# Kernel tuning notes

Measured on AMD Instinct MI355X. Metric: run time of the kernel, lower is better.

## Reference

```python
import jax, jax.numpy as jnp
import numpy as np

B, NV, NQ, NA = 128, 100, 14, 10
V_DIM, Q_DIM, A_DIM = 2048, 1024, 1024
H_DIM, RANK, HD, G = 512, 32, 16, 2  # HD = H_DIM // RANK, G = glimpse


def setup_inputs() -> dict:
    key = jax.random.key(0)
    ks = jax.random.split(key, 16)
    s = 0.05
    return {
        "v": jax.random.normal(ks[0], (B, NV, V_DIM), jnp.float32),
        "q": jax.random.normal(ks[1], (B, NQ, Q_DIM), jnp.float32),
        "a": jax.random.normal(ks[2], (B, NA, A_DIM), jnp.float32),
        # tucker projections (FCNet = Linear + ReLU; dropout identity at eval)
        "Wv": jax.random.normal(ks[3], (H_DIM, V_DIM), jnp.float32) * s,
        "bv": jnp.zeros((H_DIM,), jnp.float32),
        "Wq": jax.random.normal(ks[4], (H_DIM, Q_DIM), jnp.float32) * s,
        "bq": jnp.zeros((H_DIM,), jnp.float32),
        "Wa": jax.random.normal(ks[5], (H_DIM, A_DIM), jnp.float32) * s,
        "ba": jnp.zeros((H_DIM,), jnp.float32),
        # rank-wise projection nets, stacked over rank: [rank, HD, H_DIM]
        "Wvr": jax.random.normal(ks[6], (RANK, HD, H_DIM), jnp.float32) * s,
        "bvr": jnp.zeros((RANK, HD), jnp.float32),
        "Wqr": jax.random.normal(ks[7], (RANK, HD, H_DIM), jnp.float32) * s,
        "bqr": jnp.zeros((RANK, HD), jnp.float32),
        "War": jax.random.normal(ks[8], (RANK, HD, H_DIM), jnp.float32) * s,
        "bar": jnp.zeros((RANK, HD), jnp.float32),
        # Tucker core T_g with h_out squeezed: [rank, hv, hq, ha, glimpse]
        "T": jax.random.normal(ks[9], (RANK, HD, HD, HD, G), jnp.float32),
    }


def reference(v, q, a, Wv, bv, Wq, bq, Wa, ba, Wvr, bvr, Wqr, bqr, War, bar, T):
    relu = jax.nn.relu
    # modality tucker projections: [B, N, H_DIM]
    vt = relu(jnp.einsum('bnd,hd->bnh', v, Wv) + bv)
    qt = relu(jnp.einsum('bnd,hd->bnh', q, Wq) + bq)
    at = relu(jnp.einsum('bnd,hd->bnh', a, Wa) + ba)
    # rank-wise FCNets, batched over rank: [B, rank, N, HD]
    v_ = relu(jnp.einsum('bnh,rch->brnc', vt, Wvr) + bvr[None, :, None, :])
    q_ = relu(jnp.einsum('bnh,rch->brnc', qt, Wqr) + bqr[None, :, None, :])
    a_ = relu(jnp.einsum('bnh,rch->brnc', at, War) + bar[None, :, None, :])
    # 6-way Tucker contraction, summed over rank: [B, NV, NQ, NA, G]
    f_emb = jnp.einsum('rijkg,bnvi,bnqj,bnak->bvqag', T, v_, q_, a_,
                       optimize=True)
    return f_emb
```

## Files before the change

### kernel.cpp

```cpp
#include <hip/hip_runtime.h>
#include <cstddef>
#include <cstdint>

#define B_    128
#define NV_   100
#define NQ_   14
#define NA_   10
#define HDIM  512
#define RANK_ 32
#define HD_   16
#define G_    2

typedef __bf16 bf16x8 __attribute__((ext_vector_type(8)));
typedef float  f32x4  __attribute__((ext_vector_type(4)));
union Frag { uint4 u; bf16x8 v; };

__device__ __forceinline__ unsigned int f2bf(float f) {
  unsigned int u = __float_as_uint(f);
  u = (u + 0x7FFFu + ((u >> 16) & 1u)) >> 16;
  return u & 0xFFFFu;
}

__device__ __forceinline__ void gload_lds16(const unsigned short* gp,
                                            unsigned short* dp) {
  __builtin_amdgcn_global_load_lds(
      (const __attribute__((address_space(1))) void*)gp,
      (__attribute__((address_space(3))) void*)dp, 16, 0, 0);
}

__global__ __launch_bounds__(256) void cvt_kernel(
    const float* __restrict__ s0, const float* __restrict__ s1,
    const float* __restrict__ s2, const float* __restrict__ s3,
    const float* __restrict__ s4, const float* __restrict__ s5,
    const float* __restrict__ s6, const float* __restrict__ s7,
    unsigned short* __restrict__ dst)
{
  const int pref[8] = {896, 1536, 2048, 2304, 2560, 2688, 2816, 2944};
  const float* srcs[8] = {s0, s1, s2, s3, s4, s5, s6, s7};
  const int blk = blockIdx.x;
  int seg = 0;
  #pragma unroll
  for (int i = 0; i < 7; ++i) if (blk >= pref[i]) seg = i + 1;
  const int base_chunk = seg ? pref[seg - 1] : 0;
  const size_t loc = (size_t)(blk - base_chunk) * 2048 + threadIdx.x * 8;
  const float* s = srcs[seg] + loc;
  float4 f0 = *(const float4*)s;
  float4 f1 = *(const float4*)(s + 4);
  ushort4 o0, o1;
  o0.x = f2bf(f0.x); o0.y = f2bf(f0.y); o0.z = f2bf(f0.z); o0.w = f2bf(f0.w);
  o1.x = f2bf(f1.x); o1.y = f2bf(f1.y); o1.z = f2bf(f1.z); o1.w = f2bf(f1.w);
  unsigned short* d = dst + (size_t)blk * 2048 + threadIdx.x * 8;
  *(ushort4*)d = o0;
  *(ushort4*)(d + 4) = o1;
}

__device__ __forceinline__ void stage_swz8(const unsigned short* __restrict__ src,
                                           int K, unsigned short* dst, int t)
{
  const int wb = t & 448;
  const int l = t & 63;
  #pragma unroll
  for (int i = 0; i < 2; ++i) {
    const int sb = i * 512 + wb;
    const int li = sb + l;
    const int row = li >> 3;
    const int p = li & 7;
    const int s = p ^ (row & 7);
    gload_lds16(src + (size_t)row * K + s * 8, dst + sb * 8);
  }
}

__device__ __forceinline__ void cvt_write(const float4 f[4], unsigned short* Abuf,
                                          int ar, int kq)
{
  unsigned short* base = Abuf + ar * 64;
  #pragma unroll
  for (int j = 0; j < 2; ++j) {
    uint4 p;
    p.x = f2bf(f[2*j].x)   | (f2bf(f[2*j].y)   << 16);
    p.y = f2bf(f[2*j].z)   | (f2bf(f[2*j].w)   << 16);
    p.z = f2bf(f[2*j+1].x) | (f2bf(f[2*j+1].y) << 16);
    p.w = f2bf(f[2*j+1].z) | (f2bf(f[2*j+1].w) << 16);
    const int s = (kq * 2 + j) ^ (ar & 7);
    *(uint4*)&base[s * 8] = p;
  }
}

__global__ __launch_bounds__(512, 4) void l1_gemm(
    const float* __restrict__ v,
    const unsigned short* __restrict__ qb, const unsigned short* __restrict__ ab,
    const unsigned short* __restrict__ Wvb, const unsigned short* __restrict__ Wqb,
    const unsigned short* __restrict__ Wab,
    const float* __restrict__ bv, const float* __restrict__ bq,
    const float* __restrict__ ba,
    unsigned short* __restrict__ vtb, unsigned short* __restrict__ qtb,
    unsigned short* __restrict__ atb)
{
  __shared__ __align__(16) unsigned short As[2][8192];
  __shared__ __align__(16) unsigned short Bs[2][8192];
  const int bx = blockIdx.x;
  int grp, gx, gy, K;
  const unsigned short *A16 = qb, *W;
  const float* bias;
  unsigned short* C;
  if (bx < 400) {
    grp = 0; const int xcd = bx & 7, j = bx >> 3; const int m = xcd * 50 + j;
    gy = m >> 2; gx = m & 3; W = Wvb; bias = bv; C = vtb; K = 2048;
  } else if (bx < 456) {
    grp = 1; const int lo = bx - 400; gy = lo >> 2; gx = lo & 3;
    A16 = qb; W = Wqb; bias = bq; C = qtb; K = 1024;
  } else {
    grp = 2; const int lo = bx - 456; gy = lo >> 2; gx = lo & 3;
    A16 = ab; W = Wab; bias = ba; C = atb; K = 1024;
  }
  const int nsteps = K >> 6;
  const int bm = gy * 128, bn = gx * 128;
  const int t = threadIdx.x;
  const int w = t >> 6, l = t & 63;
  const int wm = (w >> 2) * 64, wn = (w & 3) * 32;

  f32x4 acc[4][2];
  #pragma unroll
  for (int i = 0; i < 4; ++i)
    #pragma unroll
    for (int j = 0; j < 2; ++j) acc[i][j] = f32x4{0.f, 0.f, 0.f, 0.f};

  const int ar = t >> 2, kq = t & 3;
  const float* vrow = (grp == 0)
      ? v + (size_t)(bm + ar) * 2048 + kq * 16 : (const float*)nullptr;
  float4 R0[4], R1[4];

  stage_swz8(W + (size_t)bn * K, K, Bs[0], t);
  if (grp == 0) {
    #pragma unroll
    for (int i = 0; i < 4; ++i) R0[i] = ((const float4*)vrow)[i];
    #pragma unroll
    for (int i = 0; i < 4; ++i) R1[i] = ((const float4*)(vrow + 64))[i];
    cvt_write(R0, As[0], ar, kq);
  } else {
    stage_swz8(A16 + (size_t)bm * K, K, As[0], t);
  }
  __syncthreads();

  for (int step = 0; step < nsteps; ++step) {
    const int db = step & 1;
    const bool hn = (step + 1) < nsteps;
    if (hn) stage_swz8(W + (size_t)bn * K + (step + 1) * 64, K, Bs[db ^ 1], t);
    if (grp == 0) {
      if (step + 2 < nsteps) {
        const float* p = vrow + (step + 2) * 64;
        if (db == 0) {
          #pragma unroll
          for (int i = 0; i < 4; ++i) R0[i] = ((const float4*)p)[i];
        } else {
          #pragma unroll
          for (int i = 0; i < 4; ++i) R1[i] = ((const float4*)p)[i];
        }
      }
      if (hn) {
        if (db == 0) cvt_write(R1, As[1], ar, kq);
        else         cvt_write(R0, As[0], ar, kq);
      }
    } else if (hn) {
      stage_swz8(A16 + (size_t)bm * K + (step + 1) * 64, K, As[db ^ 1], t);
    }
    const unsigned short* Ad = As[db];
    const unsigned short* Bd = Bs[db];
    #pragma unroll
    for (int ks = 0; ks < 2; ++ks) {
      Frag fa[4], fb[2];
      #pragma unroll
      for (int i = 0; i < 4; ++i) {
        const int r = wm + 16 * i + (l & 15);
        fa[i].u = *(const uint4*)&Ad[r * 64 + (((ks * 4 + (l >> 4)) ^ (r & 7)) * 8)];
      }
      #pragma unroll
      for (int j = 0; j < 2; ++j) {
        const int r = wn + 16 * j + (l & 15);
        fb[j].u = *(const uint4*)&Bd[r * 64 + (((ks * 4 + (l >> 4)) ^ (r & 7)) * 8)];
      }
      #pragma unroll
      for (int i = 0; i < 4; ++i)
        #pragma unroll
        for (int j = 0; j < 2; ++j)
          acc[i][j] = __builtin_amdgcn_mfma_f32_16x16x32_bf16(fa[i].v, fb[j].v, acc[i][j], 0, 0, 0);
    }
    __syncthreads();
  }

  const int q4 = (l >> 4) * 4, cl = l & 15;
  #pragma unroll
  for (int i = 0; i < 4; ++i)
    #pragma unroll
    for (int j = 0; j < 2; ++j) {
      const int col = bn + wn + 16 * j + cl;
      const float bs = bias[col];
      #pragma unroll
      for (int r = 0; r < 4; ++r) {
        const int row = bm + wm + 16 * i + q4 + r;
        float o = fmaxf(acc[i][j][r] + bs, 0.f);
        C[(size_t)row * 512 + col] = (unsigned short)f2bf(o);
      }
    }
}

__global__ __launch_bounds__(512, 4) void l2_gemm(
    const unsigned short* __restrict__ vtb, const unsigned short* __restrict__ qtb,
    const unsigned short* __restrict__ atb,
    const unsigned short* __restrict__ Wvrb, const unsigned short* __restrict__ Wqrb,
    const unsigned short* __restrict__ Warb,
    const float* __restrict__ bvr, const float* __restrict__ bqr,
    const float* __restrict__ bar,
    unsigned short* __restrict__ vrb, float* __restrict__ q_r, float* __restrict__ a_r)
{
  __shared__ __align__(16) unsigned short As[2][8192];
  __shared__ __align__(16) unsigned short Bs[2][8192];
  const int bx = blockIdx.x;
  int grp, gx, gy;
  const unsigned short *A16, *W;
  const float* bias;
  if (bx < 400) {
    grp = 0; const int xcd = bx & 7, j = bx >> 3; const int m = xcd * 50 + j;
    gy = m >> 2; gx = m & 3; A16 = vtb; W = Wvrb; bias = bvr;
  } else if (bx < 456) {
    grp = 1; const int lo = bx - 400; gy = lo >> 2; gx = lo & 3;
    A16 = qtb; W = Wqrb; bias = bqr;
  } else {
    grp = 2; const int lo = bx - 456; gy = lo >> 2; gx = lo & 3;
    A16 = atb; W = Warb; bias = bar;
  }
  const int bm = gy * 128, bn = gx * 128;
  const int t = threadIdx.x;
  const int w = t >> 6, l = t & 63;
  const int wm = (w >> 2) * 64, wn = (w & 3) * 32;

  f32x4 acc[4][2];
  #pragma unroll
  for (int i = 0; i < 4; ++i)
    #pragma unroll
    for (int j = 0; j < 2; ++j) acc[i][j] = f32x4{0.f, 0.f, 0.f, 0.f};

  stage_swz8(W + (size_t)bn * 512, 512, Bs[0], t);
  stage_swz8(A16 + (size_t)bm * 512, 512, As[0], t);
  __syncthreads();

  for (int step = 0; step < 8; ++step) {
    const int db = step & 1;
    const bool hn = (step + 1) < 8;
    const int k0n = (step + 1) << 6;
    if (hn) {
      stage_swz8(W + (size_t)bn * 512 + k0n, 512, Bs[db ^ 1], t);
      stage_swz8(A16 + (size_t)bm * 512 + k0n, 512, As[db ^ 1], t);
    }
    const unsigned short* Ad = As[db];
    const unsigned short* Bd = Bs[db];
    #pragma unroll
    for (int ks = 0; ks < 2; ++ks) {
      Frag fa[4], fb[2];
      #pragma unroll
      for (int i = 0; i < 4; ++i) {
        const int r = wm + 16 * i + (l & 15);
        fa[i].u = *(const uint4*)&Ad[r * 64 + (((ks * 4 + (l >> 4)) ^ (r & 7)) * 8)];
      }
      #pragma unroll
      for (int j = 0; j < 2; ++j) {
        const int r = wn + 16 * j + (l & 15);
        fb[j].u = *(const uint4*)&Bd[r * 64 + (((ks * 4 + (l >> 4)) ^ (r & 7)) * 8)];
      }
      #pragma unroll
      for (int i = 0; i < 4; ++i)
        #pragma unroll
        for (int j = 0; j < 2; ++j)
          acc[i][j] = __builtin_amdgcn_mfma_f32_16x16x32_bf16(fa[i].v, fb[j].v, acc[i][j], 0, 0, 0);
    }
    __syncthreads();
  }

  const int q4 = (l >> 4) * 4, cl = l & 15;
  #pragma unroll
  for (int i = 0; i < 4; ++i)
    #pragma unroll
    for (int j = 0; j < 2; ++j) {
      const int col = bn + wn + 16 * j + cl;
      const float bs = bias[col];
      #pragma unroll
      for (int r = 0; r < 4; ++r) {
        const int row = bm + wm + 16 * i + q4 + r;
        float o = fmaxf(acc[i][j][r] + bs, 0.f);
        if (grp == 0)      vrb[(size_t)row * 512 + col] = (unsigned short)f2bf(o);
        else if (grp == 1) q_r[(size_t)row * 512 + col] = o;
        else               a_r[(size_t)row * 512 + col] = o;
      }
    }
}

__global__ void tsum_kernel(const float* __restrict__ T, float* __restrict__ Tsum)
{
  const int idx = blockIdx.x * 256 + threadIdx.x;
  float s = 0.f;
  #pragma unroll
  for (int r = 0; r < RANK_; ++r) s += T[r * 8192 + idx];
  Tsum[idx] = s;
}

__global__ __launch_bounds__(256) void build_w_kernel(
    const float* __restrict__ q_, const float* __restrict__ a_,
    const float* __restrict__ Tsum, unsigned short* __restrict__ WmatT)
{
  const int n = blockIdx.x, b = blockIdx.y, t = threadIdx.x;
  __shared__ float Ts[8192];
  __shared__ float U[14 * 544];

  #pragma unroll
  for (int s = 0; s < 8; ++s)
    ((float4*)Ts)[s * 256 + t] = ((const float4*)Tsum)[s * 256 + t];
  __syncthreads();

  {
    const int i = t >> 4, k = t & 15;
    float acc0[NQ_], acc1[NQ_];
    #pragma unroll
    for (int q = 0; q < NQ_; ++q) { acc0[q] = 0.f; acc1[q] = 0.f; }
    const float* qbase = q_ + (size_t)b * NQ_ * HDIM + n * 16;
    #pragma unroll
    for (int j = 0; j < 16; ++j) {
      float2 ts = *(const float2*)&Ts[i * 512 + j * 32 + k * 2];
      #pragma unroll
      for (int q = 0; q < NQ_; ++q) {
        float qv = qbase[q * HDIM + j];
        acc0[q] += ts.x * qv;
        acc1[q] += ts.y * qv;
      }
    }
    #pragma unroll
    for (int q = 0; q < NQ_; ++q) {
      float2 uu; uu.x = acc0[q]; uu.y = acc1[q];
      *(float2*)&U[q * 544 + i * 34 + k * 2] = uu;
    }
  }
  __syncthreads();

  if ((t >> 4) < NQ_) {
    const int q = t >> 4, i = t & 15;
    float acc0[NA_], acc1[NA_];
    #pragma unroll
    for (int a = 0; a < NA_; ++a) { acc0[a] = 0.f; acc1[a] = 0.f; }
    const float* abase = a_ + (size_t)b * NA_ * HDIM + n * 16;
    #pragma unroll
    for (int k = 0; k < 16; ++k) {
      float2 uu = *(const float2*)&U[q * 544 + i * 34 + k * 2];
      #pragma unroll
      for (int a = 0; a < NA_; ++a) {
        float av = abase[a * HDIM + k];
        acc0[a] += uu.x * av;
        acc1[a] += uu.y * av;
      }
    }
    unsigned short* wb = WmatT + (size_t)b * 320 * 512 + (n * 16 + i);
    #pragma unroll
    for (int a = 0; a < NA_; ++a) {
      wb[(size_t)((q * 10 + a) * 2 + 0) * 512] = (unsigned short)f2bf(acc0[a]);
      wb[(size_t)((q * 10 + a) * 2 + 1) * 512] = (unsigned short)f2bf(acc1[a]);
    }
  }
}

__device__ __forceinline__ void final_stage(
    const unsigned short* __restrict__ Vrb, const unsigned short* __restrict__ Wb,
    int b, int mh, int n0, int k0, int t,
    unsigned short* Asb, unsigned short* Bsb)
{
  const int w = t >> 6, l = t & 63;
  {
    int grow = b * NV_ + mh * 64 + w * 16 + (l >> 2);
    if (grow > B_ * NV_ - 1) grow = B_ * NV_ - 1;
    gload_lds16(Vrb + (size_t)grow * HDIM + k0 + (l & 3) * 8, &Asb[w * 512]);
  }
  #pragma unroll
  for (int c = 0; c < 3; ++c) {
    const int base = c * 256 + w * 64;
    if (base < 640) {
      const int li = base + l;
      const int nrow = li >> 2, ko2 = (li & 3) * 8;
      gload_lds16(Wb + (size_t)(n0 + nrow) * 512 + k0 + ko2, &Bsb[base * 8]);
    }
  }
}

__global__ __launch_bounds__(256) void final_mfma(
    const unsigned short* __restrict__ Vrb, const unsigned short* __restrict__ WmatT,
    float* __restrict__ out)
{
  __shared__ __align__(16) unsigned short As[2][2048];
  __shared__ __align__(16) unsigned short Bs[2][5120];
  const int b  = blockIdx.y;
  const int mh = blockIdx.x >> 1;
  const int n0 = (blockIdx.x & 1) * 160;
  const int t = threadIdx.x;
  const int w = t >> 6, l = t & 63;
  const int wm = (w >> 1) * 32;
  const int wn = (w & 1) * 80;

  f32x4 acc[2][5];
  #pragma unroll
  for (int mi = 0; mi < 2; ++mi)
    #pragma unroll
    for (int nj = 0; nj < 5; ++nj) acc[mi][nj] = f32x4{0.f, 0.f, 0.f, 0.f};

  const unsigned short* Wb = WmatT + (size_t)b * 320 * 512;

  final_stage(Vrb, Wb, b, mh, n0, 0, t, As[0], Bs[0]);
  __syncthreads();

  for (int step = 0; step < 16; ++step) {
    const int db = step & 1;
    if (step + 1 < 16)
      final_stage(Vrb, Wb, b, mh, n0, (step + 1) * 32, t, As[db ^ 1], Bs[db ^ 1]);

    Frag fa[2], fb[5];
    #pragma unroll
    for (int mi = 0; mi < 2; ++mi)
      fa[mi].u = *(const uint4*)&As[db][(wm + mi * 16 + (l & 15)) * 32 + (l >> 4) * 8];
    #pragma unroll
    for (int nj = 0; nj < 5; ++nj)
      fb[nj].u = *(const uint4*)&Bs[db][(wn + nj * 16 + (l & 15)) * 32 + (l >> 4) * 8];
    #pragma unroll
    for (int mi = 0; mi < 2; ++mi)
      #pragma unroll
      for (int nj = 0; nj < 5; ++nj)
        acc[mi][nj] = __builtin_amdgcn_mfma_f32_16x16x32_bf16(fa[mi].v, fb[nj].v, acc[mi][nj], 0, 0, 0);
    __syncthreads();
  }

  #pragma unroll
  for (int mi = 0; mi < 2; ++mi)
    #pragma unroll
    for (int nj = 0; nj < 5; ++nj) {
      const int col = n0 + wn + nj * 16 + (l & 15);
      if (col < 280) {
        #pragma unroll
        for (int r = 0; r < 4; ++r) {
          const int row = mh * 64 + wm + mi * 16 + (l >> 4) * 4 + r;
          if (row < NV_)
            out[((size_t)b * NV_ + row) * 280 + col] = acc[mi][nj][r];
        }
      }
    }
}

extern "C" void kernel_launch(void* const* d_in, const int* in_sizes, int n_in,
                              void* d_out, int out_size, void* d_ws, size_t ws_size,
                              hipStream_t stream)
{
  const float* v   = (const float*)d_in[0];
  const float* q   = (const float*)d_in[1];
  const float* a   = (const float*)d_in[2];
  const float* Wv  = (const float*)d_in[3];
  const float* bv  = (const float*)d_in[4];
  const float* Wq  = (const float*)d_in[5];
  const float* bq  = (const float*)d_in[6];
  const float* Wa  = (const float*)d_in[7];
  const float* ba  = (const float*)d_in[8];
  const float* Wvr = (const float*)d_in[9];
  const float* bvr = (const float*)d_in[10];
  const float* Wqr = (const float*)d_in[11];
  const float* bqr = (const float*)d_in[12];
  const float* War = (const float*)d_in[13];
  const float* bar = (const float*)d_in[14];
  const float* T   = (const float*)d_in[15];

  unsigned short* wsu = (unsigned short*)d_ws;
  float* wsf = (float*)d_ws;

  unsigned short* WmatT = wsu;
  unsigned short* qb    = wsu;
  unsigned short* ab    = wsu + 1835008;
  unsigned short* Wvb   = wsu + 3145728;
  unsigned short* Wqb   = wsu + 4194304;
  unsigned short* Wab   = wsu + 4718592;
  unsigned short* Wvrb  = wsu + 5242880;
  unsigned short* Wqrb  = wsu + 5505024;
  unsigned short* Warb  = wsu + 5767168;
  unsigned short* vtb   = wsu + 20971520;
  unsigned short* qtb   = wsu + 27525120;
  unsigned short* atb   = wsu + 28442624;
  unsigned short* vrb   = wsu + 29097984;
  float* q_r  = wsf + 17825792;
  float* a_r  = wsf + 18743296;
  float* Tsum = wsf + 19398656;

  cvt_kernel<<<2944, 256, 0, stream>>>(q, a, Wv, Wq, Wa, Wvr, Wqr, War, wsu);

  l1_gemm<<<496, 512, 0, stream>>>(v, qb, ab, Wvb, Wqb, Wab, bv, bq, ba,
                                   vtb, qtb, atb);
  l2_gemm<<<496, 512, 0, stream>>>(vtb, qtb, atb, Wvrb, Wqrb, Warb,
                                   bvr, bqr, bar, vrb, q_r, a_r);

  tsum_kernel<<<32, 256, 0, stream>>>(T, Tsum);
  build_w_kernel<<<dim3(32, 128), 256, 0, stream>>>(q_r, a_r, Tsum, WmatT);
  final_mfma<<<dim3(4, 128), 256, 0, stream>>>(vrb, WmatT, (float*)d_out);
}
```

Baseline: 328.0 us.

## Fold Tsum into convert kernel and deepen final GEMM K tile with swizzle

The rank-summation of T moves into extra blocks of the conversion kernel, which removes one kernel launch. The final MFMA kernel doubles its K tile from 32 to 64 and halves the loop trip count. It also stages tiles with an XOR-swizzled layout to cut LDS bank conflicts on fragment reads, and adds an occupancy hint in launch bounds. The cost is twice the shared memory per block, which may lower how many blocks fit on a CU.

```diff
diff --git a/kernel.cpp b/kernel.cpp
--- a/kernel.cpp
+++ b/kernel.cpp
@@ -33,11 +33,20 @@
     const float* __restrict__ s2, const float* __restrict__ s3,
     const float* __restrict__ s4, const float* __restrict__ s5,
     const float* __restrict__ s6, const float* __restrict__ s7,
-    unsigned short* __restrict__ dst)
-{
+    unsigned short* __restrict__ dst,
+    const float* __restrict__ T, float* __restrict__ Tsum)
+{
+  const int blk = blockIdx.x;
+  if (blk >= 2944) {
+    const int idx = (blk - 2944) * 256 + threadIdx.x;
+    float s = 0.f;
+    #pragma unroll
+    for (int r = 0; r < RANK_; ++r) s += T[r * 8192 + idx];
+    Tsum[idx] = s;
+    return;
+  }
   const int pref[8] = {896, 1536, 2048, 2304, 2560, 2688, 2816, 2944};
   const float* srcs[8] = {s0, s1, s2, s3, s4, s5, s6, s7};
-  const int blk = blockIdx.x;
   int seg = 0;
   #pragma unroll
   for (int i = 0; i < 7; ++i) if (blk >= pref[i]) seg = i + 1;
@@ -210,7 +219,7 @@
     const unsigned short* __restrict__ Wvrb, const unsigned short* __restrict__ Wqrb,
     const unsigned short* __restrict__ Warb,
     const float* __restrict__ bvr, const float* __restrict__ bqr,
-    const float* __restrict__ bar,
+    const float* __restrict__ bar_,
     unsigned short* __restrict__ vrb, float* __restrict__ q_r, float* __restrict__ a_r)
 {
   __shared__ __align__(16) unsigned short As[2][8192];
@@ -227,7 +236,7 @@
     A16 = qtb; W = Wqrb; bias = bqr;
   } else {
     grp = 2; const int lo = bx - 456; gy = lo >> 2; gx = lo & 3;
-    A16 = atb; W = Warb; bias = bar;
+    A16 = atb; W = Warb; bias = bar_;
   }
   const int bm = gy * 128, bn = gx * 128;
   const int t = threadIdx.x;
@@ -294,15 +303,6 @@
     }
 }
 
-__global__ void tsum_kernel(const float* __restrict__ T, float* __restrict__ Tsum)
-{
-  const int idx = blockIdx.x * 256 + threadIdx.x;
-  float s = 0.f;
-  #pragma unroll
-  for (int r = 0; r < RANK_; ++r) s += T[r * 8192 + idx];
-  Tsum[idx] = s;
-}
-
 __global__ __launch_bounds__(256) void build_w_kernel(
     const float* __restrict__ q_, const float* __restrict__ a_,
     const float* __restrict__ Tsum, unsigned short* __restrict__ WmatT)
@@ -365,39 +365,18 @@
   }
 }
 
-__device__ __forceinline__ void final_stage(
-    const unsigned short* __restrict__ Vrb, const unsigned short* __restrict__ Wb,
-    int b, int mh, int n0, int k0, int t,
-    unsigned short* Asb, unsigned short* Bsb)
-{
-  const int w = t >> 6, l = t & 63;
-  {
-    int grow = b * NV_ + mh * 64 + w * 16 + (l >> 2);
-    if (grow > B_ * NV_ - 1) grow = B_ * NV_ - 1;
-    gload_lds16(Vrb + (size_t)grow * HDIM + k0 + (l & 3) * 8, &Asb[w * 512]);
-  }
-  #pragma unroll
-  for (int c = 0; c < 3; ++c) {
-    const int base = c * 256 + w * 64;
-    if (base < 640) {
-      const int li = base + l;
-      const int nrow = li >> 2, ko2 = (li & 3) * 8;
-      gload_lds16(Wb + (size_t)(n0 + nrow) * 512 + k0 + ko2, &Bsb[base * 8]);
-    }
-  }
-}
-
-__global__ __launch_bounds__(256) void final_mfma(
+__global__ __launch_bounds__(256, 2) void final_mfma(
     const unsigned short* __restrict__ Vrb, const unsigned short* __restrict__ WmatT,
     float* __restrict__ out)
 {
-  __shared__ __align__(16) unsigned short As[2][2048];
-  __shared__ __align__(16) unsigned short Bs[2][5120];
+  __shared__ __align__(16) unsigned short As[2][4096];
+  __shared__ __align__(16) unsigned short Bs[2][10240];
   const int b  = blockIdx.y;
   const int mh = blockIdx.x >> 1;
   const int n0 = (blockIdx.x & 1) * 160;
   const int t = threadIdx.x;
   const int w = t >> 6, l = t & 63;
+  const int wb = w * 64;
   const int wm = (w >> 1) * 32;
   const int wn = (w & 1) * 80;
 
@@ -409,28 +388,59 @@
 
   const unsigned short* Wb = WmatT + (size_t)b * 320 * 512;
 
-  final_stage(Vrb, Wb, b, mh, n0, 0, t, As[0], Bs[0]);
+  #define FINAL_STAGE(k0, Asb, Bsb)                                          \
+    {                                                                        \
+      _Pragma("unroll")                                                      \
+      for (int i = 0; i < 2; ++i) {                                          \
+        const int sb = i * 256 + wb;                                         \
+        const int li = sb + l;                                               \
+        const int row = li >> 3, s = (li & 7) ^ (row & 7);                   \
+        int grow = b * NV_ + mh * 64 + row;                                  \
+        if (grow > B_ * NV_ - 1) grow = B_ * NV_ - 1;                        \
+        gload_lds16(Vrb + (size_t)grow * 512 + (k0) + s * 8, (Asb) + sb * 8);\
+      }                                                                      \
+      _Pragma("unroll")                                                      \
+      for (int i = 0; i < 5; ++i) {                                          \
+        const int sb = i * 256 + wb;                                         \
+        const int li = sb + l;                                               \
+        const int row = li >> 3, s = (li & 7) ^ (row & 7);                   \
+        gload_lds16(Wb + (size_t)(n0 + row) * 512 + (k0) + s * 8,            \
+                    (Bsb) + sb * 8);                                         \
+      }                                                                      \
+    }
+
+  FINAL_STAGE(0, As[0], Bs[0]);
   __syncthreads();
 
-  for (int step = 0; step < 16; ++step) {
+  for (int step = 0; step < 8; ++step) {
     const int db = step & 1;
-    if (step + 1 < 16)
-      final_stage(Vrb, Wb, b, mh, n0, (step + 1) * 32, t, As[db ^ 1], Bs[db ^ 1]);
-
-    Frag fa[2], fb[5];
-    #pragma unroll
-    for (int mi = 0; mi < 2; ++mi)
-      fa[mi].u = *(const uint4*)&As[db][(wm + mi * 16 + (l & 15)) * 32 + (l >> 4) * 8];
-    #pragma unroll
-    for (int nj = 0; nj < 5; ++nj)
-      fb[nj].u = *(const uint4*)&Bs[db][(wn + nj * 16 + (l & 15)) * 32 + (l >> 4) * 8];
-    #pragma unroll
-    for (int mi = 0; mi < 2; ++mi)
-      #pragma unroll
-      for (int nj = 0; nj < 5; ++nj)
-        acc[mi][nj] = __builtin_amdgcn_mfma_f32_16x16x32_bf16(fa[mi].v, fb[nj].v, acc[mi][nj], 0, 0, 0);
+    if (step + 1 < 8)
+      FINAL_STAGE((step + 1) * 64, As[db ^ 1], Bs[db ^ 1]);
+
+    const unsigned short* Ad = As[db];
+    const unsigned short* Bd = Bs[db];
+    #pragma unroll
+    for (int ks = 0; ks < 2; ++ks) {
+      Frag fa[2], fb[5];
+      #pragma unroll
+      for (int mi = 0; mi < 2; ++mi) {
+        const int r = wm + mi * 16 + (l & 15);
+        fa[mi].u = *(const uint4*)&Ad[r * 64 + (((ks * 4 + (l >> 4)) ^ (r & 7)) * 8)];
+      }
+      #pragma unroll
+      for (int nj = 0; nj < 5; ++nj) {
+        const int r = wn + nj * 16 + (l & 15);
+        fb[nj].u = *(const uint4*)&Bd[r * 64 + (((ks * 4 + (l >> 4)) ^ (r & 7)) * 8)];
+      }
+      #pragma unroll
+      for (int mi = 0; mi < 2; ++mi)
+        #pragma unroll
+        for (int nj = 0; nj < 5; ++nj)
+          acc[mi][nj] = __builtin_amdgcn_mfma_f32_16x16x32_bf16(fa[mi].v, fb[nj].v, acc[mi][nj], 0, 0, 0);
+    }
     __syncthreads();
   }
+  #undef FINAL_STAGE
 
   #pragma unroll
   for (int mi = 0; mi < 2; ++mi)
@@ -489,14 +499,14 @@
   float* a_r  = wsf + 18743296;
   float* Tsum = wsf + 19398656;
 
-  cvt_kernel<<<2944, 256, 0, stream>>>(q, a, Wv, Wq, Wa, Wvr, Wqr, War, wsu);
+  cvt_kernel<<<2976, 256, 0, stream>>>(q, a, Wv, Wq, Wa, Wvr, Wqr, War, wsu,
+                                       T, Tsum);
 
   l1_gemm<<<496, 512, 0, stream>>>(v, qb, ab, Wvb, Wqb, Wab, bv, bq, ba,
                                    vtb, qtb, atb);
   l2_gemm<<<496, 512, 0, stream>>>(vtb, qtb, atb, Wvrb, Wqrb, Warb,
                                    bvr, bqr, bar, vrb, q_r, a_r);
 
-  tsum_kernel<<<32, 256, 0, stream>>>(T, Tsum);
   build_w_kernel<<<dim3(32, 128), 256, 0, stream>>>(q_r, a_r, Tsum, WmatT);
   final_mfma<<<dim3(4, 128), 256, 0, stream>>>(vrb, WmatT, (float*)d_out);
 }
```

Result: no change. 325.3 us (-0.8%).
